# Kernel optimization log

Hardware: AMD Instinct MI355X
Metric: run time of the kernel (lower is better)

## Reference

```python
import jax, jax.numpy as jnp
import numpy as np

PAD = [(1, 1), (1, 1), (1, 1)]
DN = ('NCDHW', 'OIDHW', 'NCDHW')


def conv3d(x, w):
    # x: [B,Ci,D,H,W], w: [Co,Ci,3,3,3], stride 1, pad 1 (BasicConv3d, bn=False, bias=False)
    return jax.lax.conv_general_dilated(x, w, (1, 1, 1), PAD, dimension_numbers=DN)


def deconv3d(x, w):
    # torch ConvTranspose3d weight [Ci,Co,3,3,3], stride 1, pad 1 == conv with spatially flipped kernel
    wf = jnp.flip(w, axis=(2, 3, 4)).transpose(1, 0, 2, 3, 4)
    return conv3d(x, wf)


def sru_dir(X, Wx, F, R, reverse):
    # SRU linear recurrence over the spectral axis (dim 2).
    # t=0: C = 1 - f_0 (faithful to SRUconvLayer's Ct-is-None branch)
    # t>0: C = f*C + (1-f)*Wx ;  h = r*C + (1-r)*x
    mt = lambda a: jnp.moveaxis(a, 2, 0)  # [T,B,C,H,W]
    x, w, f, r = mt(X), mt(Wx), mt(F), mt(R)
    if reverse:
        x, w, f, r = x[::-1], w[::-1], f[::-1], r[::-1]
    C0 = 1.0 - f[0]
    h0 = r[0] * C0 + (1.0 - r[0]) * x[0]

    def step(C, inp):
        x_, w_, f_, r_ = inp
        Cn = f_ * C + (1.0 - f_) * w_
        return Cn, r_ * Cn + (1.0 - r_) * x_

    _, hs = jax.lax.scan(step, C0, (x[1:], w[1:], f[1:], r[1:]))
    h = jnp.concatenate([h0[None], hs], axis=0)
    if reverse:
        h = h[::-1]
    return jnp.moveaxis(h, 0, 2)


def do_sru(x, w, deconv=False):
    # DoSRUconv: 6-way gate split, bidirectional scan (ft/rt forward, ft2/rt2 backward), sum
    g = deconv3d(x, w) if deconv else conv3d(x, w)
    Wx, ft, ft2, rt, rt2, X = jnp.split(g, 6, axis=1)
    Wx = jnp.tanh(Wx)
    X = jnp.tanh(X)  # act == 'tanh'
    ft, ft2, rt, rt2 = (jax.nn.sigmoid(a) for a in (ft, ft2, rt, rt2))
    return sru_dir(X, Wx, ft, rt, False) + sru_dir(X, Wx, ft2, rt2, True)


def si_sru(x, w, reverse, deconv=False):
    # SiSRUconv: 4-way gate split, single-direction scan
    g = deconv3d(x, w) if deconv else conv3d(x, w)
    Wx, ft, rt, X = jnp.split(g, 4, axis=1)
    return sru_dir(jnp.tanh(X), jnp.tanh(Wx), jax.nn.sigmoid(ft), jax.nn.sigmoid(rt), reverse)


def nssnn_forward(x, w_head, w_e0, w_e1, w_d0, w_d1, w_tail):
    h = do_sru(x, w_head)                                 # head: 1 -> 16, bidirectional
    e0 = si_sru(h, w_e0, reverse=False)                   # encoder: 16 -> 32 (alt direction)
    e1 = si_sru(e0, w_e1, reverse=True)                   # encoder: 32 -> 64
    d0 = si_sru(e1, w_d0, reverse=False, deconv=True) + e0  # decoder: 64 -> 32, skip add
    d1 = si_sru(d0, w_d1, reverse=True, deconv=True) + h    # decoder: 32 -> 16, skip add
    out = do_sru(d1, w_tail, deconv=True)                 # tail: 16 -> 1, bidirectional
    return out + x                                        # global residual


def setup_inputs() -> dict:
    key = jax.random.key(0)
    ks = jax.random.split(key, 7)
    B, Cin, Ch, D, H, W = 1, 1, 16, 31, 96, 96
    s = 0.05
    x = jax.random.normal(ks[0], (B, Cin, D, H, W), dtype=jnp.float32)
    w_head = jax.random.normal(ks[1], (6 * Ch, Cin, 3, 3, 3), dtype=jnp.float32) * s
    w_e0 = jax.random.normal(ks[2], (4 * 2 * Ch, Ch, 3, 3, 3), dtype=jnp.float32) * s
    w_e1 = jax.random.normal(ks[3], (4 * 4 * Ch, 2 * Ch, 3, 3, 3), dtype=jnp.float32) * s
    # ConvTranspose3d weights: [Cin, Cout, 3,3,3]
    w_d0 = jax.random.normal(ks[4], (4 * Ch, 4 * 2 * Ch, 3, 3, 3), dtype=jnp.float32) * s
    w_d1 = jax.random.normal(ks[5], (2 * Ch, 4 * Ch, 3, 3, 3), dtype=jnp.float32) * s
    w_tail = jax.random.normal(ks[6], (Ch, 6 * Cin, 3, 3, 3), dtype=jnp.float32) * s
    return {"x": x, "w_head": w_head, "w_e0": w_e0, "w_e1": w_e1,
            "w_d0": w_d0, "w_d1": w_d1, "w_tail": w_tail}


def reference(x, w_head, w_e0, w_e1, w_d0, w_d1, w_tail):
    return nssnn_forward(x, w_head, w_e0, w_e1, w_d0, w_d1, w_tail)
```

## Files before the change

kernel.cpp:

```cpp
#include <hip/hip_runtime.h>
#include <hip/hip_bf16.h>


#define D_DIM 31
#define H_DIM 96
#define W_DIM 96
#define HW (H_DIM * W_DIM)
#define SVOX (D_DIM * HW)

typedef __hip_bfloat16 bf16;
typedef __attribute__((ext_vector_type(8))) short short8;
typedef __attribute__((ext_vector_type(4))) short short4a;
typedef __attribute__((ext_vector_type(4))) float f32x4;

__device__ __forceinline__ float sigm(float v) { return 1.0f / (1.0f + __expf(-v)); }
__device__ __forceinline__ short f2bs(float v) {
    bf16 h = __float2bfloat16(v);
    return *(short*)&h;
}
__device__ __forceinline__ float bs2f(short s) {
    return __uint_as_float(((unsigned)(unsigned short)s) << 16);
}

template <typename T> __device__ __forceinline__ float ldf(const T* p);
template <> __device__ __forceinline__ float ldf<float>(const float* p) { return *p; }
template <> __device__ __forceinline__ float ldf<bf16>(const bf16* p) {
    return __bfloat162float(*p);
}
template <typename T> __device__ __forceinline__ void stf(T* p, float v);
template <> __device__ __forceinline__ void stf<float>(float* p, float v) { *p = v; }
template <> __device__ __forceinline__ void stf<bf16>(bf16* p, float v) {
    *p = __float2bfloat16(v);
}

#define P8 ((size_t)8 * SVOX)

__global__ __launch_bounds__(256) void wtrans_all_k(const float* __restrict__ w_e0,
                                                    const float* __restrict__ w_e1,
                                                    const float* __restrict__ w_d0,
                                                    const float* __restrict__ w_d1,
                                                    const float* __restrict__ w_tail,
                                                    bf16* __restrict__ wt) {
    int i = blockIdx.x * 256 + threadIdx.x;
    if (i >= 635904) return;
    if (i >= 608256) {
        int j = i - 608256;
        int ci = j % 32;
        int r = j / 32;
        int oc_c = r & 31;
        int kk = (r >> 5) % 27;
        float v = 0.0f;
        if (ci < 16 && oc_c < 6)
            v = w_tail[(ci * 6 + oc_c) * 27 + (26 - kk)];
        wt[i] = __float2bfloat16(v);
        return;
    }
    const float* w;
    int j, C_in, C_out_w, Ch, deconv, cip;
    if (i < 110592)      { w = w_e0; j = i;          C_in = 16; C_out_w = 128; Ch = 32; deconv = 0; cip = 32; }
    else if (i < 331776) { w = w_e1; j = i - 110592; C_in = 32; C_out_w = 256; Ch = 64; deconv = 0; cip = 32; }
    else if (i < 552960) { w = w_d0; j = i - 331776; C_in = 64; C_out_w = 128; Ch = 32; deconv = 1; cip = 64; }
    else                 { w = w_d1; j = i - 552960; C_in = 32; C_out_w = 64;  Ch = 16; deconv = 1; cip = 32; }
    int ci = j % cip;
    int r = j / cip;
    int oc_c = r & 31; r >>= 5;
    int kk = r % 27;
    int chunk = r / 27;
    int oc_w = (oc_c >> 3) * Ch + chunk * 8 + (oc_c & 7);
    float v = 0.0f;
    if (ci < C_in)
        v = deconv ? w[((size_t)ci * C_out_w + oc_w) * 27 + (26 - kk)]
                   : w[((size_t)oc_w * C_in + ci) * 27 + kk];
    wt[i] = __float2bfloat16(v);
}

template <int CI32, int NT, int EPI>
__global__ __launch_bounds__(256) void conv_mfma_k(const bf16* __restrict__ x,
                                                   const bf16* __restrict__ wt,
                                                   bf16* __restrict__ g, int C_in) {
    constexpr int RS = 34;
    constexpr int CIP = CI32 * 32;
    __shared__ short row[6 * 98 * RS];

    const int t = threadIdx.x;
    const int lane = t & 63, wave = t >> 6;
    const int l15 = lane & 15, g4 = lane >> 4;
    const int h0 = blockIdx.x * 4, d = blockIdx.y;
    const short* xs = (const short*)x;

    f32x4 acc[6][NT];
#pragma unroll
    for (int m = 0; m < 6; ++m)
#pragma unroll
        for (int n = 0; n < NT; ++n) acc[m][n] = (f32x4){0.f, 0.f, 0.f, 0.f};

    for (int kd = 0; kd < 3; ++kd) {
        const int dd = d + kd - 1;
        if ((unsigned)dd >= D_DIM) continue;
        for (int cb = 0; cb < CI32; ++cb) {
            __syncthreads();
            for (int i = t; i < 98 * 6 * 4; i += 256) {
                int wp = i % 98;
                int j = i / 98;
                int hl = j % 6;
                int cg = j / 6;
                int hh = h0 + hl - 1;
                int gw = wp - 1;
                const int cblk = cb * 4 + cg;
                short8 v = {0, 0, 0, 0, 0, 0, 0, 0};
                if ((unsigned)hh < H_DIM && (unsigned)gw < W_DIM && cblk * 8 < C_in)
                    v = *(const short8*)(xs + (size_t)cblk * P8 +
                                         ((size_t)dd * HW + hh * W_DIM + gw) * 8);
                *(short8*)(row + ((size_t)hl * 98 + wp) * RS + cg * 8) = v;
            }
            __syncthreads();

            const bf16* wa = wt + (size_t)l15 * CIP + cb * 32 + g4 * 8;
#pragma unroll
            for (int kh = 0; kh < 3; ++kh) {
#pragma unroll
                for (int kw = 0; kw < 3; ++kw) {
                    const int kk = (kd * 3 + kh) * 3 + kw;
                    const size_t arow = (size_t)kk * 32 * CIP;
                    short8 a0 = *(const short8*)(wa + arow);
                    short8 a1;
                    if (NT == 2) a1 = *(const short8*)(wa + arow + (size_t)16 * CIP);
                    const int boff = ((wave + kh) * 98 + l15 + kw) * RS + g4 * 8;
#pragma unroll
                    for (int m = 0; m < 6; ++m) {
                        short8 b = *(const short8*)(row + boff + (m * 16) * RS);
                        acc[m][0] = __builtin_amdgcn_mfma_f32_16x16x32_bf16(a0, b, acc[m][0], 0, 0, 0);
                        if (NT == 2)
                            acc[m][1] = __builtin_amdgcn_mfma_f32_16x16x32_bf16(a1, b, acc[m][1], 0, 0, 0);
                    }
                }
            }
        }
    }

    const int hy = h0 + wave;
    short* gs = (short*)g;
#pragma unroll
    for (int m = 0; m < 6; ++m) {
        const int wx = m * 16 + l15;
        const size_t dhw = (size_t)d * HW + hy * W_DIM + wx;
        if (EPI == 0) {
#pragma unroll
            for (int n = 0; n < NT; ++n) {
                const int gate = n * 2 + (g4 >> 1);
                const bool th = (gate == 0 || gate == 3);
                short4a pack;
#pragma unroll
                for (int r = 0; r < 4; ++r) {
                    float a = acc[m][n][r];
                    pack[r] = f2bs(th ? tanhf(a) : sigm(a));
                }
                *(short4a*)(gs + (size_t)gate * P8 + dhw * 8 + (g4 & 1) * 4) = pack;
            }
        } else {
#pragma unroll
            for (int r = 0; r < 4; ++r) {
                const int oc = g4 * 4 + r;
                if (oc < 6) {
                    float a = acc[m][0][r];
                    const bool th = (oc == 0 || oc == 5);
                    stf(g + (size_t)oc * SVOX + dhw, th ? tanhf(a) : sigm(a));
                }
            }
        }
    }
}

__global__ __launch_bounds__(256) void head_conv_k(const float* __restrict__ x,
                                                   const float* __restrict__ w,
                                                   bf16* __restrict__ g) {
    __shared__ float tile[3][34][36];
    __shared__ float wsh[8 * 27];

    const int t = threadIdx.x;
    const int lx = t & 15;
    const int ly = t >> 4;
    const int tbx = (blockIdx.x % 3) * 32;
    const int tby = (blockIdx.x / 3) * 32;
    const int d = blockIdx.y;
    const int bz = blockIdx.z;
    const int gate = bz >> 1;
    const int ocw0 = gate * 16 + (bz & 1) * 8;

    if (t < 8 * 27) wsh[t] = w[(ocw0 + t / 27) * 27 + (t % 27)];

    for (int i = t; i < 3 * 34 * 34; i += 256) {
        int dz = i / 1156;
        int rem = i - dz * 1156;
        int r = rem / 34;
        int c = rem - r * 34;
        int gd = d + dz - 1;
        int gy = tby + r - 1;
        int gx = tbx + c - 1;
        float v = 0.0f;
        if ((unsigned)gd < D_DIM && (unsigned)gy < H_DIM && (unsigned)gx < W_DIM)
            v = x[((size_t)gd * H_DIM + gy) * W_DIM + gx];
        tile[dz][r][c] = v;
    }
    __syncthreads();

    float acc[8][4];
#pragma unroll
    for (int o = 0; o < 8; ++o)
#pragma unroll
        for (int p = 0; p < 4; ++p) acc[o][p] = 0.0f;

#pragma unroll
    for (int kd = 0; kd < 3; ++kd)
#pragma unroll
        for (int kh = 0; kh < 3; ++kh) {
            float wv[8][3];
#pragma unroll
            for (int o = 0; o < 8; ++o)
#pragma unroll
                for (int kw = 0; kw < 3; ++kw)
                    wv[o][kw] = wsh[o * 27 + (kd * 3 + kh) * 3 + kw];
            const int r0 = ly * 2 + kh;
            float v0[4], v1[4];
#pragma unroll
            for (int c = 0; c < 4; ++c) {
                v0[c] = tile[kd][r0][lx * 2 + c];
                v1[c] = tile[kd][r0 + 1][lx * 2 + c];
            }
#pragma unroll
            for (int kw = 0; kw < 3; ++kw)
#pragma unroll
                for (int o = 0; o < 8; ++o) {
                    acc[o][0] = fmaf(v0[kw],     wv[o][kw], acc[o][0]);
                    acc[o][1] = fmaf(v0[kw + 1], wv[o][kw], acc[o][1]);
                    acc[o][2] = fmaf(v1[kw],     wv[o][kw], acc[o][2]);
                    acc[o][3] = fmaf(v1[kw + 1], wv[o][kw], acc[o][3]);
                }
        }

    const bool th = (gate == 0 || gate == 5);
    const int hy = tby + ly * 2, wx = tbx + lx * 2;
    short* gs = (short*)g;
#pragma unroll
    for (int p = 0; p < 4; ++p) {
        const int py = hy + (p >> 1), px = wx + (p & 1);
        short8 pack;
#pragma unroll
        for (int o = 0; o < 8; ++o) {
            float a = acc[o][p];
            pack[o] = f2bs(th ? tanhf(a) : sigm(a));
        }
        *(short8*)(gs + (size_t)bz * P8 + ((size_t)d * HW + py * W_DIM + px) * 8) = pack;
    }
}

template <int REV>
__global__ __launch_bounds__(256) void si_sru_scan_k(const bf16* __restrict__ g,
                                                     const bf16* __restrict__ resid,
                                                     bf16* __restrict__ out, int outblk) {
    const int idx = blockIdx.x * 256 + threadIdx.x;
    const int c = idx & 7;
    const size_t hw = (size_t)(idx >> 3);
    const size_t ob = (size_t)outblk * P8;

    float C = 0.0f;
#pragma unroll
    for (int i = 0; i < D_DIM; ++i) {
        const int d = REV ? (D_DIM - 1 - i) : i;
        const size_t off = ((size_t)d * HW + hw) * 8 + c;
        float f = ldf(g + P8 + off);
        float r = ldf(g + 2 * P8 + off);
        float xv = ldf(g + 3 * P8 + off);
        float wv = ldf(g + off);
        C = (i == 0) ? (1.0f - f) : (f * C + (1.0f - f) * wv);
        float hv = r * C + (1.0f - r) * xv;
        float o = hv + (resid ? ldf(resid + ob + off) : 0.0f);
        stf(out + ob + off, o);
    }
}

__global__ __launch_bounds__(256) void do_sru_scan_k(const bf16* __restrict__ g,
                                                     bf16* __restrict__ out) {
    const int j = blockIdx.x * 256 + threadIdx.x;
    const int c = j & 7;
    const size_t hw = (size_t)(j >> 3);
    const int chb = blockIdx.y;
    const bf16* gb = g + (size_t)chb * P8;

    float hbuf[D_DIM];
    float C = 0.0f;
#pragma unroll
    for (int d = 0; d < D_DIM; ++d) {
        const size_t off = ((size_t)d * HW + hw) * 8 + c;
        float f = ldf(gb + 2 * P8 + off);
        float r = ldf(gb + 6 * P8 + off);
        float xv = ldf(gb + 10 * P8 + off);
        float wv = ldf(gb + off);
        C = (d == 0) ? (1.0f - f) : (f * C + (1.0f - f) * wv);
        hbuf[d] = r * C + (1.0f - r) * xv;
    }
#pragma unroll
    for (int i = 0; i < D_DIM; ++i) {
        const int d = D_DIM - 1 - i;
        const size_t off = ((size_t)d * HW + hw) * 8 + c;
        float f = ldf(gb + 4 * P8 + off);
        float r = ldf(gb + 8 * P8 + off);
        float xv = ldf(gb + 10 * P8 + off);
        float wv = ldf(gb + off);
        C = (i == 0) ? (1.0f - f) : (f * C + (1.0f - f) * wv);
        hbuf[d] += r * C + (1.0f - r) * xv;
    }
#pragma unroll
    for (int d = 0; d < D_DIM; ++d)
        stf(out + (size_t)chb * P8 + ((size_t)d * HW + hw) * 8 + c, hbuf[d]);
}

__global__ __launch_bounds__(256) void do_sru_final_k(const bf16* __restrict__ g,
                                                      const float* __restrict__ x,
                                                      float* __restrict__ out) {
    const size_t hw = (size_t)(blockIdx.x * 256 + threadIdx.x);

    float hbuf[D_DIM];
    float C = 0.0f;
#pragma unroll
    for (int d = 0; d < D_DIM; ++d) {
        const size_t off = (size_t)d * HW + hw;
        float f = ldf(g + SVOX + off);
        float r = ldf(g + 3 * (size_t)SVOX + off);
        float xv = ldf(g + 5 * (size_t)SVOX + off);
        float wv = ldf(g + off);
        C = (d == 0) ? (1.0f - f) : (f * C + (1.0f - f) * wv);
        hbuf[d] = r * C + (1.0f - r) * xv;
    }
#pragma unroll
    for (int i = 0; i < D_DIM; ++i) {
        const int d = D_DIM - 1 - i;
        const size_t off = (size_t)d * HW + hw;
        float f = ldf(g + 2 * (size_t)SVOX + off);
        float r = ldf(g + 4 * (size_t)SVOX + off);
        float xv = ldf(g + 5 * (size_t)SVOX + off);
        float wv = ldf(g + off);
        C = (i == 0) ? (1.0f - f) : (f * C + (1.0f - f) * wv);
        hbuf[d] += r * C + (1.0f - r) * xv + x[off];
    }
#pragma unroll
    for (int d = 0; d < D_DIM; ++d) out[(size_t)d * HW + hw] = hbuf[d];
}

extern "C" void kernel_launch(void* const* d_in, const int* in_sizes, int n_in,
                              void* d_out, int out_size, void* d_ws, size_t ws_size,
                              hipStream_t stream) {
    const float* x      = (const float*)d_in[0];
    const float* w_head = (const float*)d_in[1];
    const float* w_e0   = (const float*)d_in[2];
    const float* w_e1   = (const float*)d_in[3];
    const float* w_d0   = (const float*)d_in[4];
    const float* w_d1   = (const float*)d_in[5];
    const float* w_tail = (const float*)d_in[6];
    float* out = (float*)d_out;

    bf16* g  = (bf16*)d_ws;
    bf16* wt = g + (size_t)32 * SVOX;
    bf16* E1 = g + (size_t)48 * SVOX;
    bf16* E0 = g + (size_t)112 * SVOX;
    bf16* H  = g + (size_t)144 * SVOX;
    bf16* D0 = E0;
    bf16* D1 = E1;

    dim3 blk(256);
    const dim3 sg8(8 * 36);
    const dim3 mg(H_DIM / 4, D_DIM);

    head_conv_k<<<dim3(9, 31, 12), blk, 0, stream>>>(x, w_head, g);
    do_sru_scan_k<<<dim3(288, 2), blk, 0, stream>>>(g, H);
    wtrans_all_k<<<dim3((635904 + 255) / 256), blk, 0, stream>>>(w_e0, w_e1, w_d0, w_d1, w_tail, wt);

    for (int c = 0; c < 4; ++c) {
        conv_mfma_k<1, 2, 0><<<mg, blk, 0, stream>>>(H, wt + (size_t)c * 27648, g, 16);
        si_sru_scan_k<0><<<sg8, blk, 0, stream>>>(g, (const bf16*)nullptr, E0, c);
    }
    for (int c = 0; c < 8; ++c) {
        conv_mfma_k<1, 2, 0><<<mg, blk, 0, stream>>>(E0, wt + 110592 + (size_t)c * 27648, g, 32);
        si_sru_scan_k<1><<<sg8, blk, 0, stream>>>(g, (const bf16*)nullptr, E1, c);
    }
    for (int c = 0; c < 4; ++c) {
        conv_mfma_k<2, 2, 0><<<mg, blk, 0, stream>>>(E1, wt + 331776 + (size_t)c * 55296, g, 64);
        si_sru_scan_k<0><<<sg8, blk, 0, stream>>>(g, E0, D0, c);
    }
    for (int c = 0; c < 2; ++c) {
        conv_mfma_k<1, 2, 0><<<mg, blk, 0, stream>>>(D0, wt + 552960 + (size_t)c * 27648, g, 32);
        si_sru_scan_k<1><<<sg8, blk, 0, stream>>>(g, H, D1, c);
    }
    conv_mfma_k<1, 1, 1><<<mg, blk, 0, stream>>>(D1, wt + 608256, g, 16);
    do_sru_final_k<<<dim3(36), blk, 0, stream>>>(g, x, out);
}
```

Measured before the change: 1.295 ms.

## Compute two channel chunks per conv launch with NT=4 and fast tanh/sigmoid

```diff
diff --git a/kernel.cpp b/kernel.cpp
--- a/kernel.cpp
+++ b/kernel.cpp
@@ -13,13 +13,14 @@
 typedef __attribute__((ext_vector_type(4))) short short4a;
 typedef __attribute__((ext_vector_type(4))) float f32x4;
 
-__device__ __forceinline__ float sigm(float v) { return 1.0f / (1.0f + __expf(-v)); }
+__device__ __forceinline__ float rcp_f(float x) { return __builtin_amdgcn_rcpf(x); }
+__device__ __forceinline__ float sigm(float v) { return rcp_f(1.0f + __expf(-v)); }
+__device__ __forceinline__ float tanh_f(float v) {
+    return 1.0f - 2.0f * rcp_f(1.0f + __expf(2.0f * v));
+}
 __device__ __forceinline__ short f2bs(float v) {
     bf16 h = __float2bfloat16(v);
     return *(short*)&h;
-}
-__device__ __forceinline__ float bs2f(short s) {
-    return __uint_as_float(((unsigned)(unsigned short)s) << 16);
 }
 
 template <typename T> __device__ __forceinline__ float ldf(const T* p);
@@ -40,7 +41,7 @@
                                                     const float* __restrict__ w_d0,
                                                     const float* __restrict__ w_d1,
                                                     const float* __restrict__ w_tail,
-                                                    bf16* __restrict__ wt) {
+                                                    bf16* __restrict__ wt, int nt4) {
     int i = blockIdx.x * 256 + threadIdx.x;
     if (i >= 635904) return;
     if (i >= 608256) {
@@ -50,8 +51,7 @@
         int oc_c = r & 31;
         int kk = (r >> 5) % 27;
         float v = 0.0f;
-        if (ci < 16 && oc_c < 6)
-            v = w_tail[(ci * 6 + oc_c) * 27 + (26 - kk)];
+        if (ci < 16 && oc_c < 6) v = w_tail[(ci * 6 + oc_c) * 27 + (26 - kk)];
         wt[i] = __float2bfloat16(v);
         return;
     }
@@ -63,9 +63,18 @@
     else                 { w = w_d1; j = i - 552960; C_in = 32; C_out_w = 64;  Ch = 16; deconv = 1; cip = 32; }
     int ci = j % cip;
     int r = j / cip;
-    int oc_c = r & 31; r >>= 5;
-    int kk = r % 27;
-    int chunk = r / 27;
+    int oc_c, kk, chunk;
+    if (nt4) {
+        int oc64 = r & 63; r >>= 6;
+        kk = r % 27;
+        int grp = r / 27;
+        chunk = grp * 2 + (oc64 >> 5);
+        oc_c = oc64 & 31;
+    } else {
+        oc_c = r & 31; r >>= 5;
+        kk = r % 27;
+        chunk = r / 27;
+    }
     int oc_w = (oc_c >> 3) * Ch + chunk * 8 + (oc_c & 7);
     float v = 0.0f;
     if (ci < C_in)
@@ -77,9 +86,11 @@
 template <int CI32, int NT, int EPI>
 __global__ __launch_bounds__(256) void conv_mfma_k(const bf16* __restrict__ x,
                                                    const bf16* __restrict__ wt,
-                                                   bf16* __restrict__ g, int C_in) {
+                                                   bf16* __restrict__ g, int C_in,
+                                                   int NCH) {
     constexpr int RS = 34;
     constexpr int CIP = CI32 * 32;
+    constexpr int AROWS = (NT == 4) ? 64 : 32;
     __shared__ short row[6 * 98 * RS];
 
     const int t = threadIdx.x;
@@ -121,17 +132,17 @@
 #pragma unroll
                 for (int kw = 0; kw < 3; ++kw) {
                     const int kk = (kd * 3 + kh) * 3 + kw;
-                    const size_t arow = (size_t)kk * 32 * CIP;
-                    short8 a0 = *(const short8*)(wa + arow);
-                    short8 a1;
-                    if (NT == 2) a1 = *(const short8*)(wa + arow + (size_t)16 * CIP);
+                    short8 a[NT];
+#pragma unroll
+                    for (int n = 0; n < NT; ++n)
+                        a[n] = *(const short8*)(wa + ((size_t)kk * AROWS + n * 16) * CIP);
                     const int boff = ((wave + kh) * 98 + l15 + kw) * RS + g4 * 8;
 #pragma unroll
                     for (int m = 0; m < 6; ++m) {
                         short8 b = *(const short8*)(row + boff + (m * 16) * RS);
-                        acc[m][0] = __builtin_amdgcn_mfma_f32_16x16x32_bf16(a0, b, acc[m][0], 0, 0, 0);
-                        if (NT == 2)
-                            acc[m][1] = __builtin_amdgcn_mfma_f32_16x16x32_bf16(a1, b, acc[m][1], 0, 0, 0);
+#pragma unroll
+                        for (int n = 0; n < NT; ++n)
+                            acc[m][n] = __builtin_amdgcn_mfma_f32_16x16x32_bf16(a[n], b, acc[m][n], 0, 0, 0);
                     }
                 }
             }
@@ -147,24 +158,25 @@
         if (EPI == 0) {
 #pragma unroll
             for (int n = 0; n < NT; ++n) {
-                const int gate = n * 2 + (g4 >> 1);
+                const int cz = n >> 1;
+                const int gate = (n & 1) * 2 + (g4 >> 1);
                 const bool th = (gate == 0 || gate == 3);
                 short4a pack;
 #pragma unroll
                 for (int r = 0; r < 4; ++r) {
-                    float a = acc[m][n][r];
-                    pack[r] = f2bs(th ? tanhf(a) : sigm(a));
+                    float v = acc[m][n][r];
+                    pack[r] = f2bs(th ? tanh_f(v) : sigm(v));
                 }
-                *(short4a*)(gs + (size_t)gate * P8 + dhw * 8 + (g4 & 1) * 4) = pack;
+                *(short4a*)(gs + (size_t)(gate * NCH + cz) * P8 + dhw * 8 + (g4 & 1) * 4) = pack;
             }
         } else {
 #pragma unroll
             for (int r = 0; r < 4; ++r) {
                 const int oc = g4 * 4 + r;
                 if (oc < 6) {
-                    float a = acc[m][0][r];
+                    float v = acc[m][0][r];
                     const bool th = (oc == 0 || oc == 5);
-                    stf(g + (size_t)oc * SVOX + dhw, th ? tanhf(a) : sigm(a));
+                    stf(g + (size_t)oc * SVOX + dhw, th ? tanh_f(v) : sigm(v));
                 }
             }
         }
@@ -175,7 +187,7 @@
                                                    const float* __restrict__ w,
                                                    bf16* __restrict__ g) {
     __shared__ float tile[3][34][36];
-    __shared__ float wsh[8 * 27];
+    __shared__ float wsh[16 * 27];
 
     const int t = threadIdx.x;
     const int lx = t & 15;
@@ -183,11 +195,10 @@
     const int tbx = (blockIdx.x % 3) * 32;
     const int tby = (blockIdx.x / 3) * 32;
     const int d = blockIdx.y;
-    const int bz = blockIdx.z;
-    const int gate = bz >> 1;
-    const int ocw0 = gate * 16 + (bz & 1) * 8;
-
-    if (t < 8 * 27) wsh[t] = w[(ocw0 + t / 27) * 27 + (t % 27)];
+    const int gate = blockIdx.z;
+
+    for (int i = t; i < 16 * 27; i += 256)
+        wsh[i] = w[(gate * 16 + i / 27) * 27 + (i % 27)];
 
     for (int i = t; i < 3 * 34 * 34; i += 256) {
         int dz = i / 1156;
@@ -204,9 +215,9 @@
     }
     __syncthreads();
 
-    float acc[8][4];
-#pragma unroll
-    for (int o = 0; o < 8; ++o)
+    float acc[16][4];
+#pragma unroll
+    for (int o = 0; o < 16; ++o)
 #pragma unroll
         for (int p = 0; p < 4; ++p) acc[o][p] = 0.0f;
 
@@ -214,12 +225,6 @@
     for (int kd = 0; kd < 3; ++kd)
 #pragma unroll
         for (int kh = 0; kh < 3; ++kh) {
-            float wv[8][3];
-#pragma unroll
-            for (int o = 0; o < 8; ++o)
-#pragma unroll
-                for (int kw = 0; kw < 3; ++kw)
-                    wv[o][kw] = wsh[o * 27 + (kd * 3 + kh) * 3 + kw];
             const int r0 = ly * 2 + kh;
             float v0[4], v1[4];
 #pragma unroll
@@ -228,14 +233,24 @@
                 v1[c] = tile[kd][r0 + 1][lx * 2 + c];
             }
 #pragma unroll
-            for (int kw = 0; kw < 3; ++kw)
-#pragma unroll
-                for (int o = 0; o < 8; ++o) {
-                    acc[o][0] = fmaf(v0[kw],     wv[o][kw], acc[o][0]);
-                    acc[o][1] = fmaf(v0[kw + 1], wv[o][kw], acc[o][1]);
-                    acc[o][2] = fmaf(v1[kw],     wv[o][kw], acc[o][2]);
-                    acc[o][3] = fmaf(v1[kw + 1], wv[o][kw], acc[o][3]);
-                }
+            for (int half = 0; half < 2; ++half) {
+                float wv[8][3];
+#pragma unroll
+                for (int o = 0; o < 8; ++o)
+#pragma unroll
+                    for (int kw = 0; kw < 3; ++kw)
+                        wv[o][kw] = wsh[(half * 8 + o) * 27 + (kd * 3 + kh) * 3 + kw];
+#pragma unroll
+                for (int kw = 0; kw < 3; ++kw)
+#pragma unroll
+                    for (int o = 0; o < 8; ++o) {
+                        const int oo = half * 8 + o;
+                        acc[oo][0] = fmaf(v0[kw],     wv[o][kw], acc[oo][0]);
+                        acc[oo][1] = fmaf(v0[kw + 1], wv[o][kw], acc[oo][1]);
+                        acc[oo][2] = fmaf(v1[kw],     wv[o][kw], acc[oo][2]);
+                        acc[oo][3] = fmaf(v1[kw + 1], wv[o][kw], acc[oo][3]);
+                    }
+            }
         }
 
     const bool th = (gate == 0 || gate == 5);
@@ -244,34 +259,42 @@
 #pragma unroll
     for (int p = 0; p < 4; ++p) {
         const int py = hy + (p >> 1), px = wx + (p & 1);
-        short8 pack;
-#pragma unroll
-        for (int o = 0; o < 8; ++o) {
-            float a = acc[o][p];
-            pack[o] = f2bs(th ? tanhf(a) : sigm(a));
-        }
-        *(short8*)(gs + (size_t)bz * P8 + ((size_t)d * HW + py * W_DIM + px) * 8) = pack;
+        const size_t dhw = (size_t)d * HW + py * W_DIM + px;
+#pragma unroll
+        for (int chb = 0; chb < 2; ++chb) {
+            short8 pack;
+#pragma unroll
+            for (int u = 0; u < 8; ++u) {
+                float v = acc[chb * 8 + u][p];
+                pack[u] = f2bs(th ? tanh_f(v) : sigm(v));
+            }
+            *(short8*)(gs + (size_t)(gate * 2 + chb) * P8 + dhw * 8) = pack;
+        }
     }
 }
 
 template <int REV>
 __global__ __launch_bounds__(256) void si_sru_scan_k(const bf16* __restrict__ g,
                                                      const bf16* __restrict__ resid,
-                                                     bf16* __restrict__ out, int outblk) {
+                                                     bf16* __restrict__ out,
+                                                     int NCH, int outbase) {
     const int idx = blockIdx.x * 256 + threadIdx.x;
     const int c = idx & 7;
     const size_t hw = (size_t)(idx >> 3);
-    const size_t ob = (size_t)outblk * P8;
+    const int cz = blockIdx.y;
+    const bf16* gb = g + (size_t)cz * P8;
+    const size_t gs = (size_t)NCH * P8;
+    const size_t ob = (size_t)(outbase + cz) * P8;
 
     float C = 0.0f;
 #pragma unroll
     for (int i = 0; i < D_DIM; ++i) {
         const int d = REV ? (D_DIM - 1 - i) : i;
         const size_t off = ((size_t)d * HW + hw) * 8 + c;
-        float f = ldf(g + P8 + off);
-        float r = ldf(g + 2 * P8 + off);
-        float xv = ldf(g + 3 * P8 + off);
-        float wv = ldf(g + off);
+        float f = ldf(gb + gs + off);
+        float r = ldf(gb + 2 * gs + off);
+        float xv = ldf(gb + 3 * gs + off);
+        float wv = ldf(gb + off);
         C = (i == 0) ? (1.0f - f) : (f * C + (1.0f - f) * wv);
         float hv = r * C + (1.0f - r) * xv;
         float o = hv + (resid ? ldf(resid + ob + off) : 0.0f);
@@ -358,39 +381,72 @@
     const float* w_d1   = (const float*)d_in[5];
     const float* w_tail = (const float*)d_in[6];
     float* out = (float*)d_out;
-
-    bf16* g  = (bf16*)d_ws;
-    bf16* wt = g + (size_t)32 * SVOX;
-    bf16* E1 = g + (size_t)48 * SVOX;
-    bf16* E0 = g + (size_t)112 * SVOX;
-    bf16* H  = g + (size_t)144 * SVOX;
-    bf16* D0 = E0;
-    bf16* D1 = E1;
+    bf16* ws = (bf16*)d_ws;
 
     dim3 blk(256);
-    const dim3 sg8(8 * 36);
     const dim3 mg(H_DIM / 4, D_DIM);
-
-    head_conv_k<<<dim3(9, 31, 12), blk, 0, stream>>>(x, w_head, g);
-    do_sru_scan_k<<<dim3(288, 2), blk, 0, stream>>>(g, H);
-    wtrans_all_k<<<dim3((635904 + 255) / 256), blk, 0, stream>>>(w_e0, w_e1, w_d0, w_d1, w_tail, wt);
-
-    for (int c = 0; c < 4; ++c) {
-        conv_mfma_k<1, 2, 0><<<mg, blk, 0, stream>>>(H, wt + (size_t)c * 27648, g, 16);
-        si_sru_scan_k<0><<<sg8, blk, 0, stream>>>(g, (const bf16*)nullptr, E0, c);
-    }
-    for (int c = 0; c < 8; ++c) {
-        conv_mfma_k<1, 2, 0><<<mg, blk, 0, stream>>>(E0, wt + 110592 + (size_t)c * 27648, g, 32);
-        si_sru_scan_k<1><<<sg8, blk, 0, stream>>>(g, (const bf16*)nullptr, E1, c);
-    }
-    for (int c = 0; c < 4; ++c) {
-        conv_mfma_k<2, 2, 0><<<mg, blk, 0, stream>>>(E1, wt + 331776 + (size_t)c * 55296, g, 64);
-        si_sru_scan_k<0><<<sg8, blk, 0, stream>>>(g, E0, D0, c);
-    }
-    for (int c = 0; c < 2; ++c) {
-        conv_mfma_k<1, 2, 0><<<mg, blk, 0, stream>>>(D0, wt + 552960 + (size_t)c * 27648, g, 32);
-        si_sru_scan_k<1><<<sg8, blk, 0, stream>>>(g, H, D1, c);
-    }
-    conv_mfma_k<1, 1, 1><<<mg, blk, 0, stream>>>(D1, wt + 608256, g, 16);
-    do_sru_final_k<<<dim3(36), blk, 0, stream>>>(g, x, out);
-}
+    const size_t SA = (size_t)SVOX;
+    const size_t needA = (size_t)179 * SA * sizeof(bf16);
+
+    if (ws_size >= needA) {
+        bf16* g  = ws;
+        bf16* wt = ws + 64 * SA;
+        bf16* E1 = ws + 67 * SA;
+        bf16* E0 = ws + 131 * SA;
+        bf16* H  = ws + 163 * SA;
+        bf16* D0 = E0;
+        bf16* D1 = E1;
+
+        head_conv_k<<<dim3(9, 31, 6), blk, 0, stream>>>(x, w_head, g);
+        do_sru_scan_k<<<dim3(288, 2), blk, 0, stream>>>(g, H);
+        wtrans_all_k<<<dim3(2484), blk, 0, stream>>>(w_e0, w_e1, w_d0, w_d1, w_tail, wt, 1);
+
+        for (int grp = 0; grp < 2; ++grp) {
+            conv_mfma_k<1, 4, 0><<<mg, blk, 0, stream>>>(H, wt + (size_t)grp * 55296, g, 16, 2);
+            si_sru_scan_k<0><<<dim3(288, 2), blk, 0, stream>>>(g, (const bf16*)nullptr, E0, 2, grp * 2);
+        }
+        for (int grp = 0; grp < 4; ++grp) {
+            conv_mfma_k<1, 4, 0><<<mg, blk, 0, stream>>>(E0, wt + 110592 + (size_t)grp * 55296, g, 32, 2);
+            si_sru_scan_k<1><<<dim3(288, 2), blk, 0, stream>>>(g, (const bf16*)nullptr, E1, 2, grp * 2);
+        }
+        for (int grp = 0; grp < 2; ++grp) {
+            conv_mfma_k<2, 4, 0><<<mg, blk, 0, stream>>>(E1, wt + 331776 + (size_t)grp * 110592, g, 64, 2);
+            si_sru_scan_k<0><<<dim3(288, 2), blk, 0, stream>>>(g, E0, D0, 2, grp * 2);
+        }
+        conv_mfma_k<1, 4, 0><<<mg, blk, 0, stream>>>(D0, wt + 552960, g, 32, 2);
+        si_sru_scan_k<1><<<dim3(288, 2), blk, 0, stream>>>(g, H, D1, 2, 0);
+        conv_mfma_k<1, 1, 1><<<mg, blk, 0, stream>>>(D1, wt + 608256, g, 16, 1);
+        do_sru_final_k<<<dim3(36), blk, 0, stream>>>(g, x, out);
+    } else {
+        bf16* g  = ws;
+        bf16* wt = ws + 32 * SA;
+        bf16* E1 = ws + 48 * SA;
+        bf16* E0 = ws + 112 * SA;
+        bf16* H  = ws + 144 * SA;
+        bf16* D0 = E0;
+        bf16* D1 = E1;
+
+        head_conv_k<<<dim3(9, 31, 6), blk, 0, stream>>>(x, w_head, g);
+        do_sru_scan_k<<<dim3(288, 2), blk, 0, stream>>>(g, H);
+        wtrans_all_k<<<dim3(2484), blk, 0, stream>>>(w_e0, w_e1, w_d0, w_d1, w_tail, wt, 0);
+
+        for (int c = 0; c < 4; ++c) {
+            conv_mfma_k<1, 2, 0><<<mg, blk, 0, stream>>>(H, wt + (size_t)c * 27648, g, 16, 1);
+            si_sru_scan_k<0><<<dim3(288, 1), blk, 0, stream>>>(g, (const bf16*)nullptr, E0, 1, c);
+        }
+        for (int c = 0; c < 8; ++c) {
+            conv_mfma_k<1, 2, 0><<<mg, blk, 0, stream>>>(E0, wt + 110592 + (size_t)c * 27648, g, 32, 1);
+            si_sru_scan_k<1><<<dim3(288, 1), blk, 0, stream>>>(g, (const bf16*)nullptr, E1, 1, c);
+        }
+        for (int c = 0; c < 4; ++c) {
+            conv_mfma_k<2, 2, 0><<<mg, blk, 0, stream>>>(E1, wt + 331776 + (size_t)c * 55296, g, 64, 1);
+            si_sru_scan_k<0><<<dim3(288, 1), blk, 0, stream>>>(g, E0, D0, 1, c);
+        }
+        for (int c = 0; c < 2; ++c) {
+            conv_mfma_k<1, 2, 0><<<mg, blk, 0, stream>>>(D0, wt + 552960 + (size_t)c * 27648, g, 32, 1);
+            si_sru_scan_k<1><<<dim3(288, 1), blk, 0, stream>>>(g, H, D1, 1, c);
+        }
+        conv_mfma_k<1, 1, 1><<<mg, blk, 0, stream>>>(D1, wt + 608256, g, 16, 1);
+        do_sru_final_k<<<dim3(36), blk, 0, stream>>>(g, x, out);
+    }
+}
```

After: 1.156 ms. 1.12x faster.
